# Kernel optimization log

Measured on AMD Instinct MI355X. Metric: run time of the kernel, lower is better.

Reference implementation:

```python
import jax, jax.numpy as jnp
import numpy as np


def setup_inputs() -> dict:
    key = jax.random.key(0)
    k1, k2, k3 = jax.random.split(key, 3)
    x = jax.random.normal(k1, (8192, 2048), dtype=jnp.float32)
    w = jax.random.normal(k2, (4096, 2048), dtype=jnp.float32) * 0.02  # [out, in]
    b = jax.random.normal(k3, (4096,), dtype=jnp.float32) * 0.01
    return {"x": x, "w": w, "b": b}


def reference(x, w, b):
    # Straight-through binarization: forward uses sign(w), gradient flows as identity.
    binary_w = w + jax.lax.stop_gradient(jnp.sign(w) - w)  # [out, in], values in {-1, 0, 1}
    # F.linear: x @ W^T + b
    return jnp.einsum("ni,oi->no", x, binary_w) + b
```

## Files before the change

kernel.cpp:

```cpp
#include <hip/hip_runtime.h>
#include <hip/hip_bf16.h>
#include <stdint.h>

typedef __bf16 bf16x8 __attribute__((ext_vector_type(8)));
typedef float  f32x4  __attribute__((ext_vector_type(4)));


__device__ __forceinline__ uint32_t rn2_bf16(uint32_t lo, uint32_t hi) {
  uint32_t rlo = (lo + 0x7FFFu + ((lo >> 16) & 1u)) >> 16;
  uint32_t rhi = (hi + 0x7FFFu + ((hi >> 16) & 1u)) >> 16;
  return (rhi << 16) | (rlo & 0xFFFFu);
}

__device__ __forceinline__ uint32_t sign2_bf16(uint32_t lo, uint32_t hi) {
  uint32_t slo = (lo & 0x7FFFFFFFu) ? (0x3F80u | ((lo >> 16) & 0x8000u)) : 0u;
  uint32_t shi = (hi & 0x7FFFFFFFu) ? (0x3F80u | ((hi >> 16) & 0x8000u)) : 0u;
  return (shi << 16) | slo;
}

__device__ __forceinline__ void gl16(const void* g, void* l) {
  __builtin_amdgcn_global_load_lds(
      (const __attribute__((address_space(1))) uint32_t*)g,
      (__attribute__((address_space(3))) uint32_t*)l,
      16, 0, 0);
}


__global__ void cvt_x_bf16(const uint4* __restrict__ in, uint4* __restrict__ out, int n8) {
  int stride = gridDim.x * blockDim.x;
  for (int i = blockIdx.x * blockDim.x + threadIdx.x; i < n8; i += stride) {
    uint4 a = in[2 * i + 0];
    uint4 b = in[2 * i + 1];
    uint4 o;
    o.x = rn2_bf16(a.x, a.y);
    o.y = rn2_bf16(a.z, a.w);
    o.z = rn2_bf16(b.x, b.y);
    o.w = rn2_bf16(b.z, b.w);
    out[i] = o;
  }
}

__global__ void cvt_w_sign(const uint4* __restrict__ in, uint4* __restrict__ out, int n8) {
  int stride = gridDim.x * blockDim.x;
  for (int i = blockIdx.x * blockDim.x + threadIdx.x; i < n8; i += stride) {
    uint4 a = in[2 * i + 0];
    uint4 b = in[2 * i + 1];
    uint4 o;
    o.x = sign2_bf16(a.x, a.y);
    o.y = sign2_bf16(a.z, a.w);
    o.z = sign2_bf16(b.x, b.y);
    o.w = sign2_bf16(b.z, b.w);
    out[i] = o;
  }
}


#define BAR()   __builtin_amdgcn_s_barrier()
#define LGKM0() asm volatile("s_waitcnt lgkmcnt(0)" ::: "memory")
#define VM4()   asm volatile("s_waitcnt vmcnt(4)" ::: "memory")
#define SWZ(x)  ((x) ^ ((((x) >> 9) & 1) << 5))

__global__ __launch_bounds__(512, 2) void gemm256(
    const uint16_t* __restrict__ A,
    const uint16_t* __restrict__ B,
    const float* __restrict__ bias,
    float* __restrict__ C,
    int M, int N, int K) {
  __shared__ alignas(16) uint8_t L[131072];
  uint8_t* Lb = L;

  const int tid  = threadIdx.x;
  const int lane = tid & 63;
  const int w    = tid >> 6;
  const int wr   = w >> 2;
  const int wc   = w & 3;
  const int r16  = lane & 15;
  const int kg   = lane >> 4;

  const int nbx = N >> 8;
  const int nwg = nbx * (M >> 8);
  const int bid = blockIdx.x;
  const int swb = (bid & 7) * (nwg >> 3) + (bid >> 3);
  const size_t m0 = (size_t)(swb / nbx) << 8;
  const size_t n0 = (size_t)(swb % nbx) << 8;

  const int NT = K >> 6;
  const size_t rowB = (size_t)K * 2;

  const int o0 = (w << 10) + (lane << 4);
  const int o1 = o0 + 8192;
  const int s0 = SWZ(o0);
  const int s1 = SWZ(o1);
  const size_t g0 = (size_t)(s0 >> 7) * rowB + (s0 & 127);
  const size_t g1 = (size_t)(s1 >> 7) * rowB + (s1 & 127);
  const char* Ab = (const char*)A + m0 * rowB;
  const char* Bb = (const char*)B + n0 * rowB;
  const size_t hiO = (size_t)128 * rowB;
  const int wB = w << 10;

  const int laneA = (wr * 128 + r16) * 128 + kg * 16;
  const int laneB = (wc * 64 + r16) * 128 + kg * 16;

#define STG(LOFF, SRC) do { \
    gl16((SRC) + g0, Lb + (LOFF) + wB); \
    gl16((SRC) + g1, Lb + (LOFF) + 8192 + wB); } while (0)

#define FRA(d, mi, ks) (*reinterpret_cast<const bf16x8*>( \
    Lb + (d) * 65536 + SWZ(laneA + (mi) * 2048 + (ks) * 64)))
#define FRB(d, ni, ks) (*reinterpret_cast<const bf16x8*>( \
    Lb + (d) * 65536 + 32768 + SWZ(laneB + (ni) * 2048 + (ks) * 64)))

  f32x4 acc[8][4] = {};

#define QMFMA(AARR, BARR, MB) do { \
    __builtin_amdgcn_s_setprio(1); \
    _Pragma("unroll") \
    for (int mi2 = 0; mi2 < 4; ++mi2) \
      _Pragma("unroll") \
      for (int ni = 0; ni < 4; ++ni) \
        acc[(MB) + mi2][ni] = __builtin_amdgcn_mfma_f32_16x16x32_bf16( \
            AARR[(MB) + mi2], BARR[ni], acc[(MB) + mi2][ni], 0, 0, 0); \
    __builtin_amdgcn_s_setprio(0); } while (0)

  STG(0,      Ab);
  STG(16384,  Ab + hiO);
  STG(32768,  Bb);
  STG(49152,  Bb + hiO);
  STG(65536,  Ab + 128);
  STG(81920,  Ab + hiO + 128);
  VM4();
  BAR();

  bf16x8 a0[8], a1[8], b0[4], b1[4];
  const int T = K >> 7;
  for (int t = 0; t < T; ++t) {
    const size_t c1 = (size_t)(2 * t + 1) * 128;
    const int k2i = 2 * t + 2, k3i = 2 * t + 3;
    const size_t c2 = (size_t)(k2i < NT ? k2i : NT - 1) * 128;
    const size_t c3 = (size_t)(k3i < NT ? k3i : NT - 1) * 128;

#pragma unroll
    for (int i = 0; i < 8; ++i) a0[i] = FRA(0, i, 0);
#pragma unroll
    for (int i = 0; i < 4; ++i) b0[i] = FRB(0, i, 0);
    STG(98304, Bb + c1);
    BAR(); LGKM0();
    QMFMA(a0, b0, 0);
    BAR();

#pragma unroll
    for (int i = 0; i < 8; ++i) a1[i] = FRA(0, i, 1);
#pragma unroll
    for (int i = 0; i < 4; ++i) b1[i] = FRB(0, i, 1);
    STG(114688, Bb + hiO + c1);
    BAR(); LGKM0();
    QMFMA(a0, b0, 4);
    BAR();

    STG(0, Ab + c2);
    BAR(); LGKM0();
    QMFMA(a1, b1, 0);
    BAR();

    STG(16384, Ab + hiO + c2);
    BAR(); LGKM0();
    QMFMA(a1, b1, 4);
    VM4();
    BAR();

#pragma unroll
    for (int i = 0; i < 8; ++i) a0[i] = FRA(1, i, 0);
#pragma unroll
    for (int i = 0; i < 4; ++i) b0[i] = FRB(1, i, 0);
    STG(32768, Bb + c2);
    BAR(); LGKM0();
    QMFMA(a0, b0, 0);
    BAR();

#pragma unroll
    for (int i = 0; i < 8; ++i) a1[i] = FRA(1, i, 1);
#pragma unroll
    for (int i = 0; i < 4; ++i) b1[i] = FRB(1, i, 1);
    STG(49152, Bb + hiO + c2);
    BAR(); LGKM0();
    QMFMA(a0, b0, 4);
    BAR();

    STG(65536, Ab + c3);
    BAR(); LGKM0();
    QMFMA(a1, b1, 0);
    BAR();

    STG(81920, Ab + hiO + c3);
    BAR(); LGKM0();
    QMFMA(a1, b1, 4);
    VM4();
    BAR();
  }

#pragma unroll
  for (int ni = 0; ni < 4; ++ni) {
    const size_t col = n0 + wc * 64 + ni * 16 + r16;
    const float bv = bias[col];
#pragma unroll
    for (int mi = 0; mi < 8; ++mi) {
      const size_t row0 = m0 + wr * 128 + mi * 16 + kg * 4;
#pragma unroll
      for (int j = 0; j < 4; ++j)
        C[(row0 + j) * N + col] = acc[mi][ni][j] + bv;
    }
  }
}


__global__ __launch_bounds__(256) void gemm_bin(
    const uint16_t* __restrict__ A, const uint16_t* __restrict__ B,
    const float* __restrict__ bias, float* __restrict__ C,
    int M, int N, int K) {
  constexpr int BK = 32;
  __shared__ alignas(16) uint16_t lA[128 * BK];
  __shared__ alignas(16) uint16_t lB[128 * BK];
  const int tid = threadIdx.x;
  const int lane = tid & 63;
  const int wid = tid >> 6;
  const int wr = wid >> 1, wc = wid & 1;
  const int r16 = lane & 15, kg = lane >> 4;
  const int m0 = blockIdx.y * 128, n0 = blockIdx.x * 128;
  f32x4 acc[4][4] = {};
  for (int k0 = 0; k0 < K; k0 += BK) {
    __syncthreads();
#pragma unroll
    for (int p = 0; p < 2; ++p) {
      int idx = p * 256 + tid;
      int row = idx >> 2;
      int col = (idx & 3) * 8;
      gl16(A + (size_t)(m0 + row) * K + k0 + col, lA + p * 2048 + wid * 512);
      gl16(B + (size_t)(n0 + row) * K + k0 + col, lB + p * 2048 + wid * 512);
    }
    __syncthreads();
    bf16x8 af[4], bg[4];
#pragma unroll
    for (int i = 0; i < 4; ++i)
      af[i] = *reinterpret_cast<const bf16x8*>(lA + (wr * 64 + i * 16 + r16) * BK + kg * 8);
#pragma unroll
    for (int i = 0; i < 4; ++i)
      bg[i] = *reinterpret_cast<const bf16x8*>(lB + (wc * 64 + i * 16 + r16) * BK + kg * 8);
#pragma unroll
    for (int mi = 0; mi < 4; ++mi)
#pragma unroll
      for (int ni = 0; ni < 4; ++ni)
        acc[mi][ni] = __builtin_amdgcn_mfma_f32_16x16x32_bf16(af[mi], bg[ni], acc[mi][ni], 0, 0, 0);
  }
#pragma unroll
  for (int ni = 0; ni < 4; ++ni) {
    int col = n0 + wc * 64 + ni * 16 + r16;
    float bv = bias[col];
#pragma unroll
    for (int mi = 0; mi < 4; ++mi) {
      int row0 = m0 + wr * 64 + mi * 16 + kg * 4;
#pragma unroll
      for (int j = 0; j < 4; ++j)
        C[(size_t)(row0 + j) * N + col] = acc[mi][ni][j] + bv;
    }
  }
}

__global__ void gemm_naive(const float* __restrict__ x, const float* __restrict__ w,
                           const float* __restrict__ b, float* __restrict__ out,
                           int M, int N, int K) {
  int n = blockIdx.x * blockDim.x + threadIdx.x;
  int m = blockIdx.y;
  if (n >= N || m >= M) return;
  float acc = 0.f;
  for (int k = 0; k < K; ++k) {
    float wv = w[(size_t)n * K + k];
    float s = (wv > 0.f) ? 1.f : ((wv < 0.f) ? -1.f : 0.f);
    acc += x[(size_t)m * K + k] * s;
  }
  out[(size_t)m * N + n] = acc + b[n];
}

extern "C" void kernel_launch(void* const* d_in, const int* in_sizes, int n_in,
                              void* d_out, int out_size, void* d_ws, size_t ws_size,
                              hipStream_t stream) {
  const float* x = (const float*)d_in[0];
  const float* w = (const float*)d_in[1];
  const float* b = (const float*)d_in[2];
  float* out = (float*)d_out;

  const int N = in_sizes[2];
  const int K = in_sizes[1] / N;
  const int M = in_sizes[0] / K;

  const size_t need = ((size_t)M * K + (size_t)N * K) * sizeof(uint16_t);
  if (ws_size < need) {
    hipLaunchKernelGGL(gemm_naive, dim3((N + 255) / 256, M), dim3(256), 0, stream,
                       x, w, b, out, M, N, K);
    return;
  }

  uint16_t* Xb = (uint16_t*)d_ws;
  uint16_t* Wb = Xb + (size_t)M * K;

  hipLaunchKernelGGL(cvt_x_bf16, dim3(2048), dim3(256), 0, stream,
                     (const uint4*)x, (uint4*)Xb, (M * K) / 8);
  hipLaunchKernelGGL(cvt_w_sign, dim3(2048), dim3(256), 0, stream,
                     (const uint4*)w, (uint4*)Wb, (N * K) / 8);

  const bool big_ok = (M % 256 == 0) && (N % 256 == 0) && (K % 128 == 0) &&
                      (((M / 256) * (N / 256)) % 8 == 0);
  if (big_ok) {
    hipLaunchKernelGGL(gemm256, dim3((M / 256) * (N / 256)), dim3(512), 0, stream,
                       Xb, Wb, b, out, M, N, K);
  } else {
    hipLaunchKernelGGL(gemm_bin, dim3(N / 128, M / 128), dim3(256), 0, stream,
                       Xb, Wb, b, out, M, N, K);
  }
}
```

Measured before the change: 172.0 us.

## Merge conversion kernels into one launch and widen LDS swizzle pattern

Combines the x-to-bf16 and w-to-sign conversion kernels into a single grid-stride kernel, saving one launch and its tail. Separately, the LDS address swizzle now XORs three row bits (bits 7-9) into bits 4-6 instead of a single bit into bit 5, spreading the ds_read accesses across more banks to cut conflicts in the GEMM. The swizzle has to match both the global_load_lds writes and the fragment reads; any mismatch would give wrong results.

```diff
diff --git a/kernel.cpp b/kernel.cpp
--- a/kernel.cpp
+++ b/kernel.cpp
@@ -26,31 +26,31 @@
 }
 
 
-__global__ void cvt_x_bf16(const uint4* __restrict__ in, uint4* __restrict__ out, int n8) {
+__global__ void cvt_prep(const uint4* __restrict__ x, uint4* __restrict__ xo, int nx8,
+                         const uint4* __restrict__ w, uint4* __restrict__ wo, int nw8) {
   int stride = gridDim.x * blockDim.x;
-  for (int i = blockIdx.x * blockDim.x + threadIdx.x; i < n8; i += stride) {
-    uint4 a = in[2 * i + 0];
-    uint4 b = in[2 * i + 1];
-    uint4 o;
-    o.x = rn2_bf16(a.x, a.y);
-    o.y = rn2_bf16(a.z, a.w);
-    o.z = rn2_bf16(b.x, b.y);
-    o.w = rn2_bf16(b.z, b.w);
-    out[i] = o;
-  }
-}
-
-__global__ void cvt_w_sign(const uint4* __restrict__ in, uint4* __restrict__ out, int n8) {
-  int stride = gridDim.x * blockDim.x;
-  for (int i = blockIdx.x * blockDim.x + threadIdx.x; i < n8; i += stride) {
-    uint4 a = in[2 * i + 0];
-    uint4 b = in[2 * i + 1];
-    uint4 o;
-    o.x = sign2_bf16(a.x, a.y);
-    o.y = sign2_bf16(a.z, a.w);
-    o.z = sign2_bf16(b.x, b.y);
-    o.w = sign2_bf16(b.z, b.w);
-    out[i] = o;
+  int total = nx8 + nw8;
+  for (int i = blockIdx.x * blockDim.x + threadIdx.x; i < total; i += stride) {
+    if (i < nx8) {
+      uint4 a = x[2 * i + 0];
+      uint4 b = x[2 * i + 1];
+      uint4 o;
+      o.x = rn2_bf16(a.x, a.y);
+      o.y = rn2_bf16(a.z, a.w);
+      o.z = rn2_bf16(b.x, b.y);
+      o.w = rn2_bf16(b.z, b.w);
+      xo[i] = o;
+    } else {
+      int j = i - nx8;
+      uint4 a = w[2 * j + 0];
+      uint4 b = w[2 * j + 1];
+      uint4 o;
+      o.x = sign2_bf16(a.x, a.y);
+      o.y = sign2_bf16(a.z, a.w);
+      o.z = sign2_bf16(b.x, b.y);
+      o.w = sign2_bf16(b.z, b.w);
+      wo[j] = o;
+    }
   }
 }
 
@@ -58,7 +58,7 @@
 #define BAR()   __builtin_amdgcn_s_barrier()
 #define LGKM0() asm volatile("s_waitcnt lgkmcnt(0)" ::: "memory")
 #define VM4()   asm volatile("s_waitcnt vmcnt(4)" ::: "memory")
-#define SWZ(x)  ((x) ^ ((((x) >> 9) & 1) << 5))
+#define SWZ(x)  ((x) ^ ((((x) >> 7) & 7) << 4))
 
 __global__ __launch_bounds__(512, 2) void gemm256(
     const uint16_t* __restrict__ A,
@@ -302,9 +302,8 @@
   uint16_t* Xb = (uint16_t*)d_ws;
   uint16_t* Wb = Xb + (size_t)M * K;
 
-  hipLaunchKernelGGL(cvt_x_bf16, dim3(2048), dim3(256), 0, stream,
-                     (const uint4*)x, (uint4*)Xb, (M * K) / 8);
-  hipLaunchKernelGGL(cvt_w_sign, dim3(2048), dim3(256), 0, stream,
+  hipLaunchKernelGGL(cvt_prep, dim3(2048), dim3(256), 0, stream,
+                     (const uint4*)x, (uint4*)Xb, (M * K) / 8,
                      (const uint4*)w, (uint4*)Wb, (N * K) / 8);
 
   const bool big_ok = (M % 256 == 0) && (N % 256 == 0) && (K % 128 == 0) &&
```

After: 156.5 us. 9.0% less time.
